# Kernel tuning notes

Measured on AMD Instinct MI355X. Metric: run time of the kernel, lower is better.

Reference implementation:

```python
import jax, jax.numpy as jnp
import numpy as np

N_NODES = 100000
N_EDGES = 1600000
D_IN = 128
D_OUT = 64


def setup_inputs() -> dict:
    key = jax.random.key(0)
    k1, k2, k3, k4, k5 = jax.random.split(key, 5)
    return {
        "input_feature": jax.random.normal(k1, (N_NODES, D_IN), dtype=jnp.float32),
        "weight": jax.random.normal(k2, (D_IN, D_OUT), dtype=jnp.float32) * (1.0 / np.sqrt(D_IN)),
        "bias": jnp.zeros((D_OUT,), dtype=jnp.float32),
        "adj_row": jax.random.randint(k3, (N_EDGES,), 0, N_NODES, dtype=jnp.int32),
        "adj_col": jax.random.randint(k4, (N_EDGES,), 0, N_NODES, dtype=jnp.int32),
        "adj_val": jax.random.uniform(k5, (N_EDGES,), dtype=jnp.float32),
    }


def reference(input_feature, weight, bias, adj_row, adj_col, adj_val):
    # support = X @ W  -> [N, D_OUT]
    support = input_feature @ weight
    # sparse adjacency matmul: out[i] = sum_e adj_val[e] * support[adj_col[e]] for adj_row[e] == i
    gathered = adj_val[:, None] * support[adj_col]  # [E, D_OUT]
    out = jax.ops.segment_sum(gathered, adj_row, num_segments=N_NODES)
    return out + bias
```

## Files before the change

### kernel.cpp

```cpp
#include <hip/hip_runtime.h>

constexpr int N_NODES = 100000;
constexpr int N_EDGES = 1600000;
constexpr int D_IN  = 128;
constexpr int D_OUT = 64;

constexpr int GEMM_BLOCKS = (N_NODES + 63) / 64;
constexpr int CHUNK = 4096;
constexpr int PBLK  = (N_EDGES + CHUNK - 1) / CHUNK;
constexpr int RPB   = 128;
constexpr int NBUCK = (N_NODES + RPB - 1) / RPB;
constexpr int NBPAD = 784;
constexpr int CAP_FINE = 2432;
constexpr int ESPAN = 128;
constexpr int NSPAN = N_EDGES / ESPAN;
constexpr int WT_STRIDE = 136;

typedef unsigned long long ull;
typedef unsigned short u16;
typedef unsigned int u32;
typedef __attribute__((ext_vector_type(8))) short short8;
typedef __attribute__((ext_vector_type(4))) float floatx4;

__device__ __forceinline__ u16 f32_to_bf16_rtn(float f) {
    u32 u = __float_as_uint(f);
    u32 r = u + 0x7FFFu + ((u >> 16) & 1u);
    return (u16)(r >> 16);
}

__global__ __launch_bounds__(256) void prep_kernel(const float* __restrict__ X,
                                                   const float* __restrict__ W,
                                                   u16* __restrict__ S,
                                                   const int* __restrict__ adj_row,
                                                   u32* __restrict__ H) {
    __shared__ u16 smem[64 * WT_STRIDE];

    if (blockIdx.x >= GEMM_BLOCKS) {
        u32* cnt = (u32*)smem;
        const int b = blockIdx.x - GEMM_BLOCKS;
        const int t = threadIdx.x;
        for (int i = t; i < NBUCK; i += 256) cnt[i] = 0;
        __syncthreads();
        const int base = b * CHUNK;
        #pragma unroll
        for (int j = 0; j < CHUNK / 256; ++j) {
            int e = base + t + j * 256;
            if (e < N_EDGES) atomicAdd(&cnt[(u32)adj_row[e] >> 7], 1u);
        }
        __syncthreads();
        for (int i = t; i < NBUCK; i += 256) H[b * NBUCK + i] = cnt[i];
        return;
    }

    u16* Wt = smem;
    for (int i = threadIdx.x; i < D_IN * D_OUT; i += 256) {
        int k = i >> 6, n = i & 63;
        Wt[n * WT_STRIDE + k] = f32_to_bf16_rtn(W[i]);
    }
    __syncthreads();

    const int lane = threadIdx.x & 63;
    const int wv   = threadIdx.x >> 6;
    const int m0   = blockIdx.x * 64 + wv * 16;
    const int mr   = lane & 15;
    const int q    = lane >> 4;
    int mrow = m0 + mr; if (mrow >= N_NODES) mrow = N_NODES - 1;
    const float* xb = X + mrow * D_IN + q * 8;

    floatx4 acc0 = 0, acc1 = 0, acc2 = 0, acc3 = 0;

    #pragma unroll
    for (int kt = 0; kt < 4; ++kt) {
        float4 xa = *(const float4*)(xb + kt * 32);
        float4 xc = *(const float4*)(xb + kt * 32 + 4);
        union { short8 v; u16 u[8]; } A;
        A.u[0] = f32_to_bf16_rtn(xa.x); A.u[1] = f32_to_bf16_rtn(xa.y);
        A.u[2] = f32_to_bf16_rtn(xa.z); A.u[3] = f32_to_bf16_rtn(xa.w);
        A.u[4] = f32_to_bf16_rtn(xc.x); A.u[5] = f32_to_bf16_rtn(xc.y);
        A.u[6] = f32_to_bf16_rtn(xc.z); A.u[7] = f32_to_bf16_rtn(xc.w);

        const u16* wrow = &Wt[mr * WT_STRIDE + kt * 32 + q * 8];
        short8 b0 = *(const short8*)(wrow + 0 * 16 * WT_STRIDE);
        short8 b1 = *(const short8*)(wrow + 1 * 16 * WT_STRIDE);
        short8 b2 = *(const short8*)(wrow + 2 * 16 * WT_STRIDE);
        short8 b3 = *(const short8*)(wrow + 3 * 16 * WT_STRIDE);
        acc0 = __builtin_amdgcn_mfma_f32_16x16x32_bf16(A.v, b0, acc0, 0, 0, 0);
        acc1 = __builtin_amdgcn_mfma_f32_16x16x32_bf16(A.v, b1, acc1, 0, 0, 0);
        acc2 = __builtin_amdgcn_mfma_f32_16x16x32_bf16(A.v, b2, acc2, 0, 0, 0);
        acc3 = __builtin_amdgcn_mfma_f32_16x16x32_bf16(A.v, b3, acc3, 0, 0, 0);
    }

    #pragma unroll
    for (int reg = 0; reg < 4; ++reg) {
        int rr = m0 + q * 4 + reg;
        if (rr < N_NODES) {
            u16* sp = &S[rr * D_OUT + mr];
            sp[0]  = f32_to_bf16_rtn(acc0[reg]);
            sp[16] = f32_to_bf16_rtn(acc1[reg]);
            sp[32] = f32_to_bf16_rtn(acc2[reg]);
            sp[48] = f32_to_bf16_rtn(acc3[reg]);
        }
    }
}

__global__ __launch_bounds__(512) void scan1_kernel(u32* __restrict__ H,
                                                    u32* __restrict__ total) {
    __shared__ u32 wsum[8];
    const int k = blockIdx.x;
    const int t = threadIdx.x, lane = t & 63, w = t >> 6;
    u32 v = (t < PBLK) ? H[t * NBUCK + k] : 0;
    u32 incl = v;
    #pragma unroll
    for (int off = 1; off < 64; off <<= 1) {
        u32 u = __shfl_up(incl, off);
        if (lane >= off) incl += u;
    }
    if (lane == 63) wsum[w] = incl;
    __syncthreads();
    u32 wb = 0;
    for (int i = 0; i < w; ++i) wb += wsum[i];
    if (t < PBLK) H[t * NBUCK + k] = wb + incl - v;
    if (t == 511) total[k] = wb + incl;
}

__global__ __launch_bounds__(1024) void scan2_kernel(const u32* __restrict__ total,
                                                     u32* __restrict__ bucketStart) {
    __shared__ u32 wsum[16];
    const int t = threadIdx.x, lane = t & 63, w = t >> 6;
    u32 v = (t < NBUCK) ? total[t] : 0;
    u32 incl = v;
    #pragma unroll
    for (int off = 1; off < 64; off <<= 1) {
        u32 u = __shfl_up(incl, off);
        if (lane >= off) incl += u;
    }
    if (lane == 63) wsum[w] = incl;
    __syncthreads();
    u32 wb = 0;
    for (int i = 0; i < w; ++i) wb += wsum[i];
    if (t < NBUCK) bucketStart[t] = wb + incl - v;
    if (t == NBUCK - 1) bucketStart[NBUCK] = wb + incl;
}

__global__ __launch_bounds__(1024) void coarse_kernel(const int* __restrict__ adj_row,
                                                      const int* __restrict__ adj_col,
                                                      const float* __restrict__ adj_val,
                                                      const u32* __restrict__ H,
                                                      const u32* __restrict__ total,
                                                      const u32* __restrict__ bucketStart,
                                                      ull* __restrict__ edges) {
    __shared__ ull srt[CHUNK];
    __shared__ u32 lofs[NBPAD];
    __shared__ u32 cur[NBPAD];
    __shared__ u32 bp[NBUCK];
    __shared__ u32 wsum[4];

    const int b = blockIdx.x, t = threadIdx.x;
    const int base = b * CHUNK;
    const int nrec = (base + CHUNK <= N_EDGES) ? CHUNK : (N_EDGES - base);
    const bool last = (b == PBLK - 1);

    for (int i = t; i < NBPAD; i += 1024) {
        u32 c = 0;
        if (i < NBUCK) {
            u32 h0 = H[b * NBUCK + i];
            u32 h1 = last ? total[i] : H[(b + 1) * NBUCK + i];
            c = h1 - h0;
            bp[i] = bucketStart[i] + h0;
        }
        cur[i] = c;
    }
    __syncthreads();

    {
        const int lane = t & 63, w = t >> 6;
        u32 c0 = 0, c1 = 0, c2 = 0, c3 = 0, s = 0;
        if (t < NBPAD / 4) {
            c0 = cur[4 * t + 0]; c1 = cur[4 * t + 1];
            c2 = cur[4 * t + 2]; c3 = cur[4 * t + 3];
            s = c0 + c1 + c2 + c3;
        }
        u32 incl = s;
        #pragma unroll
        for (int off = 1; off < 64; off <<= 1) {
            u32 u = __shfl_up(incl, off);
            if (lane >= off) incl += u;
        }
        if (lane == 63 && w < 4) wsum[w] = incl;
        __syncthreads();
        if (t < NBPAD / 4) {
            u32 wb = 0;
            for (int i = 0; i < w; ++i) wb += wsum[i];
            u32 excl = wb + incl - s;
            lofs[4 * t + 0] = excl;
            lofs[4 * t + 1] = excl + c0;
            lofs[4 * t + 2] = excl + c0 + c1;
            lofs[4 * t + 3] = excl + c0 + c1 + c2;
            cur[4 * t + 0] = lofs[4 * t + 0];
            cur[4 * t + 1] = lofs[4 * t + 1];
            cur[4 * t + 2] = lofs[4 * t + 2];
            cur[4 * t + 3] = lofs[4 * t + 3];
        }
    }
    __syncthreads();

    #pragma unroll
    for (int j = 0; j < CHUNK / 1024; ++j) {
        int e = base + t + j * 1024;
        if (e < N_EDGES) {
            u32 row = (u32)adj_row[e];
            u32 p = atomicAdd(&cur[row >> 7], 1u);
            ull rec = ((ull)f32_to_bf16_rtn(adj_val[e]) << 48)
                    | ((ull)row << 17) | (u32)adj_col[e];
            srt[p] = rec;
        }
    }
    __syncthreads();

    for (int p = t; p < nrec; p += 1024) {
        ull rec = srt[p];
        u32 row = (u32)(rec >> 17) & 0x1FFFFu;
        u32 k = row >> 7;
        edges[bp[k] + (p - lofs[k])] = rec;
    }
}

__global__ __launch_bounds__(512) void fine_kernel(const u32* __restrict__ bucketStart,
                                                   ull* __restrict__ edges,
                                                   const float* __restrict__ bias,
                                                   float* __restrict__ out) {
    __shared__ ull srt[CAP_FINE];
    __shared__ u32 h[RPB], cur[RPB];
    __shared__ u32 lofs[RPB + 1];

    const int k = blockIdx.x, t = threadIdx.x;
    const int gbeg = (int)bucketStart[k], gend = (int)bucketStart[k + 1];
    const int len = gend - gbeg;

    if (t < RPB) h[t] = 0;
    __syncthreads();

    ull r[5];
    int cnt = 0;
    for (int i = t; i < len && cnt < 5; i += 512) {
        r[cnt] = edges[gbeg + i];
        atomicAdd(&h[(u32)(r[cnt] >> 17) & 127u], 1u);
        ++cnt;
    }
    __syncthreads();

    if (t < 64) {
        u32 v0 = h[t], v1 = h[t + 64];
        u32 i0 = v0;
        #pragma unroll
        for (int off = 1; off < 64; off <<= 1) {
            u32 u = __shfl_up(i0, off);
            if (t >= off) i0 += u;
        }
        u32 t0 = __shfl(i0, 63);
        u32 i1 = v1;
        #pragma unroll
        for (int off = 1; off < 64; off <<= 1) {
            u32 u = __shfl_up(i1, off);
            if (t >= off) i1 += u;
        }
        i1 += t0;
        lofs[t] = i0 - v0;
        lofs[t + 64] = i1 - v1;
        if (t == 0) lofs[RPB] = (u32)len;
    }
    __syncthreads();

    if (t < RPB) {
        cur[t] = lofs[t];
        u32 beg = (u32)gbeg + lofs[t];
        u32 end = (u32)gbeg + lofs[t + 1];
        h[t] = (beg == end) || (((beg + 127u) & ~127u) <= end);
    }
    __syncthreads();

    for (int c = 0; c < cnt; ++c) {
        u32 lrow = (u32)(r[c] >> 17) & 127u;
        u32 p = atomicAdd(&cur[lrow], 1u);
        if (p < CAP_FINE) srt[p] = r[c];
    }
    __syncthreads();

    const int lim = len < CAP_FINE ? len : CAP_FINE;
    for (int p = t; p < lim; p += 512) edges[gbeg + p] = srt[p];

    const float bv = bias[t & 63];
    const int rbase = k * RPB;
    for (int i = t; i < RPB * D_OUT; i += 512) {
        int rr = i >> 6;
        if (h[rr]) {
            int row = rbase + rr;
            if (row < N_NODES) out[row * D_OUT + (i & 63)] = bv;
        }
    }
}

__global__ __launch_bounds__(256) void gather_kernel(const ull* __restrict__ edges,
                                                     const u16* __restrict__ S,
                                                     const float* __restrict__ bias,
                                                     float* __restrict__ out) {
    const int lane = threadIdx.x & 63;
    const int wid  = __builtin_amdgcn_readfirstlane((blockIdx.x * 256 + threadIdx.x) >> 6);
    if (wid >= NSPAN) return;
    const float bv = bias[lane];

    const int e0 = wid * ESPAN;
    constexpr int BE = 16;
    constexpr int NBATCH = ESPAN / BE;

    int currow;
    {
        ull m0 = edges[e0];
        u32 lo = (u32)__builtin_amdgcn_readfirstlane((int)(u32)m0);
        u32 hi = (u32)__builtin_amdgcn_readfirstlane((int)(u32)(m0 >> 32));
        currow = (int)(((lo >> 17) | (hi << 15)) & 0x1FFFFu);
    }
    bool at_boundary = true;
    float acc = 0.f;

    #pragma unroll
    for (int b = 0; b < NBATCH; ++b) {
        const ull* ep = edges + e0 + b * BE;
        ulonglong2 q[8];
        #pragma unroll
        for (int u = 0; u < 8; ++u) q[u] = *(const ulonglong2*)(ep + 2 * u);
        ull m[BE];
        #pragma unroll
        for (int u = 0; u < 8; ++u) { m[2 * u] = q[u].x; m[2 * u + 1] = q[u].y; }

        u32 lo[BE], hi[BE];
        #pragma unroll
        for (int j = 0; j < BE; ++j) {
            lo[j] = (u32)__builtin_amdgcn_readfirstlane((int)(u32)m[j]);
            hi[j] = (u32)__builtin_amdgcn_readfirstlane((int)(u32)(m[j] >> 32));
        }

        float sv[BE];
        #pragma unroll
        for (int j = 0; j < BE; ++j) {
            u32 col = lo[j] & 0x1FFFFu;
            sv[j] = __uint_as_float((u32)S[col * D_OUT + lane] << 16);
        }

        #pragma unroll
        for (int j = 0; j < BE; ++j) {
            int r = (int)(((lo[j] >> 17) | (hi[j] << 15)) & 0x1FFFFu);
            if (r != currow) {
                if (at_boundary) atomicAdd(&out[currow * D_OUT + lane], acc);
                else             out[currow * D_OUT + lane] = acc + bv;
                currow = r; acc = 0.f; at_boundary = false;
            }
            float v = __uint_as_float(hi[j] & 0xFFFF0000u);
            acc += v * sv[j];
        }
    }
    atomicAdd(&out[currow * D_OUT + lane], acc);
}

extern "C" void kernel_launch(void* const* d_in, const int* in_sizes, int n_in,
                              void* d_out, int out_size, void* d_ws, size_t ws_size,
                              hipStream_t stream) {
    const float* X    = (const float*)d_in[0];
    const float* W    = (const float*)d_in[1];
    const float* bias = (const float*)d_in[2];
    const int*   row  = (const int*)d_in[3];
    const int*   col  = (const int*)d_in[4];
    const float* val  = (const float*)d_in[5];
    float* out = (float*)d_out;

    char* ws = (char*)d_ws;
    u16*  S      = (u16*) (ws + 0);
    ull*  edges  = (ull*) (ws + 12800000);
    u32*  H      = (u32*) (ws + 25600000);
    u32*  total  = (u32*) (ws + 26823048);
    u32*  bstart = (u32*) (ws + 26826176);

    prep_kernel  <<<GEMM_BLOCKS + PBLK, 256, 0, stream>>>(X, W, S, row, H);
    scan1_kernel <<<NBUCK, 512, 0, stream>>>(H, total);
    scan2_kernel <<<1, 1024, 0, stream>>>(total, bstart);
    coarse_kernel<<<PBLK, 1024, 0, stream>>>(row, col, val, H, total, bstart, edges);
    fine_kernel  <<<NBUCK, 512, 0, stream>>>(bstart, edges, bias, out);
    gather_kernel<<<(NSPAN + 3) / 4, 256, 0, stream>>>(edges, S, bias, out);
}
```

Measured before the change: 179.8 us.

## Replace two-level bucket sort with global per-row counting sort via atomics

Replaces the per-chunk bucket histograms, two-level scan, coarse local sort and fine per-bucket sort with a direct per-row histogram built with global atomics, a single-block scan over all rows, and a scatter that places each edge with a global atomic cursor. Bias initialisation moves into extra blocks of the scatter kernel. This cuts kernel launches and the fine-sort pass. In exchange it adds contended global atomics, uncoalesced scattered writes, and a serial single-block scan over 100k rows. Edge order within a row becomes nondeterministic.

```diff
diff --git a/kernel.cpp b/kernel.cpp
--- a/kernel.cpp
+++ b/kernel.cpp
@@ -8,13 +8,10 @@
 constexpr int GEMM_BLOCKS = (N_NODES + 63) / 64;
 constexpr int CHUNK = 4096;
 constexpr int PBLK  = (N_EDGES + CHUNK - 1) / CHUNK;
-constexpr int RPB   = 128;
-constexpr int NBUCK = (N_NODES + RPB - 1) / RPB;
-constexpr int NBPAD = 784;
-constexpr int CAP_FINE = 2432;
 constexpr int ESPAN = 128;
 constexpr int NSPAN = N_EDGES / ESPAN;
 constexpr int WT_STRIDE = 136;
+constexpr int BIAS_BLOCKS = (N_NODES + 1023) / 1024;
 
 typedef unsigned long long ull;
 typedef unsigned short u16;
@@ -32,23 +29,18 @@
                                                    const float* __restrict__ W,
                                                    u16* __restrict__ S,
                                                    const int* __restrict__ adj_row,
-                                                   u32* __restrict__ H) {
+                                                   u32* __restrict__ rowCnt) {
     __shared__ u16 smem[64 * WT_STRIDE];
 
     if (blockIdx.x >= GEMM_BLOCKS) {
-        u32* cnt = (u32*)smem;
         const int b = blockIdx.x - GEMM_BLOCKS;
         const int t = threadIdx.x;
-        for (int i = t; i < NBUCK; i += 256) cnt[i] = 0;
-        __syncthreads();
         const int base = b * CHUNK;
         #pragma unroll
         for (int j = 0; j < CHUNK / 256; ++j) {
             int e = base + t + j * 256;
-            if (e < N_EDGES) atomicAdd(&cnt[(u32)adj_row[e] >> 7], 1u);
-        }
-        __syncthreads();
-        for (int i = t; i < NBUCK; i += 256) H[b * NBUCK + i] = cnt[i];
+            if (e < N_EDGES) atomicAdd(&rowCnt[(u32)adj_row[e]], 1u);
+        }
         return;
     }
 
@@ -103,82 +95,22 @@
     }
 }
 
-__global__ __launch_bounds__(512) void scan1_kernel(u32* __restrict__ H,
-                                                    u32* __restrict__ total) {
-    __shared__ u32 wsum[8];
-    const int k = blockIdx.x;
-    const int t = threadIdx.x, lane = t & 63, w = t >> 6;
-    u32 v = (t < PBLK) ? H[t * NBUCK + k] : 0;
-    u32 incl = v;
-    #pragma unroll
-    for (int off = 1; off < 64; off <<= 1) {
-        u32 u = __shfl_up(incl, off);
-        if (lane >= off) incl += u;
-    }
-    if (lane == 63) wsum[w] = incl;
-    __syncthreads();
-    u32 wb = 0;
-    for (int i = 0; i < w; ++i) wb += wsum[i];
-    if (t < PBLK) H[t * NBUCK + k] = wb + incl - v;
-    if (t == 511) total[k] = wb + incl;
-}
-
-__global__ __launch_bounds__(1024) void scan2_kernel(const u32* __restrict__ total,
-                                                     u32* __restrict__ bucketStart) {
+__global__ __launch_bounds__(1024) void scan_rows_kernel(const u32* __restrict__ rowCnt,
+                                                         u32* __restrict__ rowStart,
+                                                         u32* __restrict__ cur) {
     __shared__ u32 wsum[16];
     const int t = threadIdx.x, lane = t & 63, w = t >> 6;
-    u32 v = (t < NBUCK) ? total[t] : 0;
-    u32 incl = v;
-    #pragma unroll
-    for (int off = 1; off < 64; off <<= 1) {
-        u32 u = __shfl_up(incl, off);
-        if (lane >= off) incl += u;
-    }
-    if (lane == 63) wsum[w] = incl;
-    __syncthreads();
-    u32 wb = 0;
-    for (int i = 0; i < w; ++i) wb += wsum[i];
-    if (t < NBUCK) bucketStart[t] = wb + incl - v;
-    if (t == NBUCK - 1) bucketStart[NBUCK] = wb + incl;
-}
-
-__global__ __launch_bounds__(1024) void coarse_kernel(const int* __restrict__ adj_row,
-                                                      const int* __restrict__ adj_col,
-                                                      const float* __restrict__ adj_val,
-                                                      const u32* __restrict__ H,
-                                                      const u32* __restrict__ total,
-                                                      const u32* __restrict__ bucketStart,
-                                                      ull* __restrict__ edges) {
-    __shared__ ull srt[CHUNK];
-    __shared__ u32 lofs[NBPAD];
-    __shared__ u32 cur[NBPAD];
-    __shared__ u32 bp[NBUCK];
-    __shared__ u32 wsum[4];
-
-    const int b = blockIdx.x, t = threadIdx.x;
-    const int base = b * CHUNK;
-    const int nrec = (base + CHUNK <= N_EDGES) ? CHUNK : (N_EDGES - base);
-    const bool last = (b == PBLK - 1);
-
-    for (int i = t; i < NBPAD; i += 1024) {
-        u32 c = 0;
-        if (i < NBUCK) {
-            u32 h0 = H[b * NBUCK + i];
-            u32 h1 = last ? total[i] : H[(b + 1) * NBUCK + i];
-            c = h1 - h0;
-            bp[i] = bucketStart[i] + h0;
-        }
-        cur[i] = c;
-    }
-    __syncthreads();
-
-    {
-        const int lane = t & 63, w = t >> 6;
-        u32 c0 = 0, c1 = 0, c2 = 0, c3 = 0, s = 0;
-        if (t < NBPAD / 4) {
-            c0 = cur[4 * t + 0]; c1 = cur[4 * t + 1];
-            c2 = cur[4 * t + 2]; c3 = cur[4 * t + 3];
-            s = c0 + c1 + c2 + c3;
+    constexpr int TILE = 8192;
+    constexpr int NT = (N_NODES + TILE - 1) / TILE;
+    u32 carry = 0;
+    for (int tile = 0; tile < NT; ++tile) {
+        const int base = tile * TILE + t * 8;
+        u32 v[8]; u32 s = 0;
+        #pragma unroll
+        for (int j = 0; j < 8; ++j) {
+            int idx = base + j;
+            v[j] = (idx < N_NODES) ? rowCnt[idx] : 0;
+            s += v[j];
         }
         u32 incl = s;
         #pragma unroll
@@ -186,117 +118,58 @@
             u32 u = __shfl_up(incl, off);
             if (lane >= off) incl += u;
         }
-        if (lane == 63 && w < 4) wsum[w] = incl;
+        if (lane == 63) wsum[w] = incl;
         __syncthreads();
-        if (t < NBPAD / 4) {
-            u32 wb = 0;
-            for (int i = 0; i < w; ++i) wb += wsum[i];
-            u32 excl = wb + incl - s;
-            lofs[4 * t + 0] = excl;
-            lofs[4 * t + 1] = excl + c0;
-            lofs[4 * t + 2] = excl + c0 + c1;
-            lofs[4 * t + 3] = excl + c0 + c1 + c2;
-            cur[4 * t + 0] = lofs[4 * t + 0];
-            cur[4 * t + 1] = lofs[4 * t + 1];
-            cur[4 * t + 2] = lofs[4 * t + 2];
-            cur[4 * t + 3] = lofs[4 * t + 3];
-        }
-    }
-    __syncthreads();
-
-    #pragma unroll
-    for (int j = 0; j < CHUNK / 1024; ++j) {
-        int e = base + t + j * 1024;
-        if (e < N_EDGES) {
-            u32 row = (u32)adj_row[e];
-            u32 p = atomicAdd(&cur[row >> 7], 1u);
-            ull rec = ((ull)f32_to_bf16_rtn(adj_val[e]) << 48)
-                    | ((ull)row << 17) | (u32)adj_col[e];
-            srt[p] = rec;
-        }
-    }
-    __syncthreads();
-
-    for (int p = t; p < nrec; p += 1024) {
-        ull rec = srt[p];
-        u32 row = (u32)(rec >> 17) & 0x1FFFFu;
-        u32 k = row >> 7;
-        edges[bp[k] + (p - lofs[k])] = rec;
-    }
-}
-
-__global__ __launch_bounds__(512) void fine_kernel(const u32* __restrict__ bucketStart,
-                                                   ull* __restrict__ edges,
-                                                   const float* __restrict__ bias,
-                                                   float* __restrict__ out) {
-    __shared__ ull srt[CAP_FINE];
-    __shared__ u32 h[RPB], cur[RPB];
-    __shared__ u32 lofs[RPB + 1];
-
-    const int k = blockIdx.x, t = threadIdx.x;
-    const int gbeg = (int)bucketStart[k], gend = (int)bucketStart[k + 1];
-    const int len = gend - gbeg;
-
-    if (t < RPB) h[t] = 0;
-    __syncthreads();
-
-    ull r[5];
-    int cnt = 0;
-    for (int i = t; i < len && cnt < 5; i += 512) {
-        r[cnt] = edges[gbeg + i];
-        atomicAdd(&h[(u32)(r[cnt] >> 17) & 127u], 1u);
-        ++cnt;
-    }
-    __syncthreads();
-
-    if (t < 64) {
-        u32 v0 = h[t], v1 = h[t + 64];
-        u32 i0 = v0;
-        #pragma unroll
-        for (int off = 1; off < 64; off <<= 1) {
-            u32 u = __shfl_up(i0, off);
-            if (t >= off) i0 += u;
-        }
-        u32 t0 = __shfl(i0, 63);
-        u32 i1 = v1;
-        #pragma unroll
-        for (int off = 1; off < 64; off <<= 1) {
-            u32 u = __shfl_up(i1, off);
-            if (t >= off) i1 += u;
-        }
-        i1 += t0;
-        lofs[t] = i0 - v0;
-        lofs[t + 64] = i1 - v1;
-        if (t == 0) lofs[RPB] = (u32)len;
-    }
-    __syncthreads();
-
-    if (t < RPB) {
-        cur[t] = lofs[t];
-        u32 beg = (u32)gbeg + lofs[t];
-        u32 end = (u32)gbeg + lofs[t + 1];
-        h[t] = (beg == end) || (((beg + 127u) & ~127u) <= end);
-    }
-    __syncthreads();
-
-    for (int c = 0; c < cnt; ++c) {
-        u32 lrow = (u32)(r[c] >> 17) & 127u;
-        u32 p = atomicAdd(&cur[lrow], 1u);
-        if (p < CAP_FINE) srt[p] = r[c];
-    }
-    __syncthreads();
-
-    const int lim = len < CAP_FINE ? len : CAP_FINE;
-    for (int p = t; p < lim; p += 512) edges[gbeg + p] = srt[p];
-
-    const float bv = bias[t & 63];
-    const int rbase = k * RPB;
-    for (int i = t; i < RPB * D_OUT; i += 512) {
-        int rr = i >> 6;
-        if (h[rr]) {
-            int row = rbase + rr;
-            if (row < N_NODES) out[row * D_OUT + (i & 63)] = bv;
-        }
+        u32 wb = 0;
+        for (int i = 0; i < w; ++i) wb += wsum[i];
+        u32 tilesum = 0;
+        for (int i = 0; i < 16; ++i) tilesum += wsum[i];
+        u32 excl = carry + wb + incl - s;
+        #pragma unroll
+        for (int j = 0; j < 8; ++j) {
+            int idx = base + j;
+            if (idx < N_NODES) { rowStart[idx] = excl; cur[idx] = excl; }
+            excl += v[j];
+        }
+        carry += tilesum;
+        __syncthreads();
+    }
+    if (t == 0) rowStart[N_NODES] = carry;
+}
+
+__global__ __launch_bounds__(1024) void scatter_kernel(const int* __restrict__ adj_row,
+                                                       const int* __restrict__ adj_col,
+                                                       const float* __restrict__ adj_val,
+                                                       u32* __restrict__ cur,
+                                                       const u32* __restrict__ rowStart,
+                                                       ull* __restrict__ edges,
+                                                       const float* __restrict__ bias,
+                                                       float* __restrict__ out) {
+    const int b = blockIdx.x, t = threadIdx.x;
+    if (b < PBLK) {
+        const int base = b * CHUNK;
+        #pragma unroll
+        for (int j = 0; j < CHUNK / 1024; ++j) {
+            int e = base + t + j * 1024;
+            if (e < N_EDGES) {
+                u32 row = (u32)adj_row[e];
+                u32 p = atomicAdd(&cur[row], 1u);
+                ull rec = ((ull)f32_to_bf16_rtn(adj_val[e]) << 48)
+                        | ((ull)row << 17) | (u32)adj_col[e];
+                edges[p] = rec;
+            }
+        }
+        return;
+    }
+    const int lane = t & 63, w = t >> 6;
+    const int rbase = (b - PBLK) * 1024;
+    const float bv = bias[lane];
+    for (int i = 0; i < 64; ++i) {
+        int row = rbase + w + 16 * i;
+        if (row >= N_NODES) break;
+        u32 beg = rowStart[row], end = rowStart[row + 1];
+        bool flag = (beg == end) || (((beg + 127u) & ~127u) <= end);
+        if (flag) out[row * D_OUT + lane] = bv;
     }
 }
 
@@ -374,16 +247,16 @@
     float* out = (float*)d_out;
 
     char* ws = (char*)d_ws;
-    u16*  S      = (u16*) (ws + 0);
-    ull*  edges  = (ull*) (ws + 12800000);
-    u32*  H      = (u32*) (ws + 25600000);
-    u32*  total  = (u32*) (ws + 26823048);
-    u32*  bstart = (u32*) (ws + 26826176);
-
-    prep_kernel  <<<GEMM_BLOCKS + PBLK, 256, 0, stream>>>(X, W, S, row, H);
-    scan1_kernel <<<NBUCK, 512, 0, stream>>>(H, total);
-    scan2_kernel <<<1, 1024, 0, stream>>>(total, bstart);
-    coarse_kernel<<<PBLK, 1024, 0, stream>>>(row, col, val, H, total, bstart, edges);
-    fine_kernel  <<<NBUCK, 512, 0, stream>>>(bstart, edges, bias, out);
-    gather_kernel<<<(NSPAN + 3) / 4, 256, 0, stream>>>(edges, S, bias, out);
-}
+    u16*  S        = (u16*) (ws + 0);
+    ull*  edges    = (ull*) (ws + 12800000);
+    u32*  rowCnt   = (u32*) (ws + 25600000);
+    u32*  rowStart = (u32*) (ws + 26000000);
+    u32*  cur      = (u32*) (ws + 26400064);
+
+    hipMemsetAsync(rowCnt, 0, N_NODES * sizeof(u32), stream);
+    prep_kernel     <<<GEMM_BLOCKS + PBLK, 256, 0, stream>>>(X, W, S, row, rowCnt);
+    scan_rows_kernel<<<1, 1024, 0, stream>>>(rowCnt, rowStart, cur);
+    scatter_kernel  <<<PBLK + BIAS_BLOCKS, 1024, 0, stream>>>(row, col, val, cur,
+                                                              rowStart, edges, bias, out);
+    gather_kernel   <<<(NSPAN + 3) / 4, 256, 0, stream>>>(edges, S, bias, out);
+}
```

Measured after the change: 454.5 us. 2.53x slower.
